# Optimization experiments

Measured on AMD Instinct MI355X. Metric: run time of the kernel, lower is better.

The kernel has to match this reference:

```python
import jax, jax.numpy as jnp
import numpy as np

RATIOS = (0.5, 1.0, 2.0)
SCALES = (8.0, 16.0, 32.0)
FEAT_STRIDE = 16
BASE_SIZE = 16.0
NMS_THRESH = 0.7
N_PRE = 6000   # pre-NMS top-k (eval-mode ProposalCreator default)
N_POST = 300   # post-NMS proposals per image (eval-mode default)
MIN_SIZE = 16.0
SCALE = 1.0


def generate_anchor_base():
    ab = np.zeros((len(RATIOS) * len(SCALES), 4), np.float32)
    for i, r in enumerate(RATIOS):
        for j, s in enumerate(SCALES):
            h = BASE_SIZE * s * np.sqrt(r)
            w = BASE_SIZE * s * np.sqrt(1.0 / r)
            ab[i * len(SCALES) + j] = [-h / 2.0, -w / 2.0, h / 2.0, w / 2.0]
    return jnp.asarray(ab)


def enumerate_shifted_anchor(anchor_base, feat_stride, H, W):
    sy = jnp.arange(H, dtype=jnp.float32) * feat_stride
    sx = jnp.arange(W, dtype=jnp.float32) * feat_stride
    sx, sy = jnp.meshgrid(sx, sy)  # row-major over (y, x), matching torch permute order
    shift = jnp.stack([sy.ravel(), sx.ravel(), sy.ravel(), sx.ravel()], axis=1)  # [K,4]
    anchors = anchor_base[None, :, :] + shift[:, None, :]  # [K, A, 4]
    return anchors.reshape(-1, 4)


def loc2bbox(anchor, loc):
    # boxes in (y1, x1, y2, x2) format
    h = anchor[:, 2] - anchor[:, 0]
    w = anchor[:, 3] - anchor[:, 1]
    cy = anchor[:, 0] + 0.5 * h
    cx = anchor[:, 1] + 0.5 * w
    dy, dx, dh, dw = loc[:, 0], loc[:, 1], loc[:, 2], loc[:, 3]
    cy = cy + dy * h
    cx = cx + dx * w
    h = h * jnp.exp(dh)
    w = w * jnp.exp(dw)
    return jnp.stack([cy - 0.5 * h, cx - 0.5 * w, cy + 0.5 * h, cx + 0.5 * w], axis=1)


def nms_fixed(boxes, scores):
    # boxes [N_PRE,4] sorted desc by scores; greedy NMS emitting N_POST picks (padded)
    area = (boxes[:, 2] - boxes[:, 0]) * (boxes[:, 3] - boxes[:, 1])

    def step(sc, _):
        i = jnp.argmax(sc)
        v = sc[i] > -jnp.inf
        b = boxes[i]
        yy1 = jnp.maximum(boxes[:, 0], b[0])
        xx1 = jnp.maximum(boxes[:, 1], b[1])
        yy2 = jnp.minimum(boxes[:, 2], b[2])
        xx2 = jnp.minimum(boxes[:, 3], b[3])
        inter = jnp.maximum(yy2 - yy1, 0.0) * jnp.maximum(xx2 - xx1, 0.0)
        iou = inter / (area + area[i] - inter + 1e-9)
        sc = jnp.where((iou > NMS_THRESH) & v, -jnp.inf, sc)
        sc = sc.at[i].set(-jnp.inf)
        return sc, (i, v)

    _, (idx, valid) = jax.lax.scan(step, scores, None, length=N_POST)
    return jnp.where(valid[:, None], boxes[idx], 0.0)  # [N_POST, 4]


def proposal_one(loc, score, anchor, img_h, img_w):
    roi = loc2bbox(anchor, loc)
    roi = jnp.stack([
        jnp.clip(roi[:, 0], 0.0, img_h), jnp.clip(roi[:, 1], 0.0, img_w),
        jnp.clip(roi[:, 2], 0.0, img_h), jnp.clip(roi[:, 3], 0.0, img_w)], axis=1)
    hs = roi[:, 2] - roi[:, 0]
    ws = roi[:, 3] - roi[:, 1]
    min_size = MIN_SIZE * SCALE
    valid = (hs >= min_size) & (ws >= min_size)
    s = jnp.where(valid, score, -jnp.inf)
    top_s, top_i = jax.lax.top_k(s, N_PRE)
    return nms_fixed(roi[top_i], top_s)


def setup_inputs() -> dict:
    key = jax.random.key(0)
    ks = jax.random.split(key, 4)
    B, C, H, W = 8, 512, 64, 64
    A = 9
    return {
        "x": jax.random.normal(ks[0], (B, C, H, W), jnp.float32),
        "conv_w": jax.random.normal(ks[1], (C, C, 3, 3), jnp.float32) * 0.01,
        "conv_b": jnp.zeros((C,), jnp.float32),
        "loc_w": jax.random.normal(ks[2], (A * 4, C, 1, 1), jnp.float32) * 0.01,
        "loc_b": jnp.zeros((A * 4,), jnp.float32),
        "cls_w": jax.random.normal(ks[3], (A * 2, C, 1, 1), jnp.float32) * 0.01,
        "cls_b": jnp.zeros((A * 2,), jnp.float32),
        "img_h": 1024,
        "img_w": 1024,
    }


def reference(x, conv_w, conv_b, loc_w, loc_b, cls_w, cls_b, img_h, img_w):
    dn = ("NCHW", "OIHW", "NCHW")
    h = jax.lax.conv_general_dilated(x, conv_w, (1, 1), "SAME", dimension_numbers=dn)
    h = jax.nn.relu(h + conv_b[None, :, None, None])
    cls = jax.nn.sigmoid(
        jax.lax.conv_general_dilated(h, cls_w, (1, 1), "VALID", dimension_numbers=dn)
        + cls_b[None, :, None, None])
    loc = (jax.lax.conv_general_dilated(h, loc_w, (1, 1), "VALID", dimension_numbers=dn)
           + loc_b[None, :, None, None])
    B, _, H, W = h.shape
    anchor = enumerate_shifted_anchor(generate_anchor_base(), FEAT_STRIDE, H, W)
    pred_locations = loc.transpose(0, 2, 3, 1).reshape(B, -1, 4)          # [B, HWA, 4]
    cls_hw = cls.transpose(0, 2, 3, 1)                                     # [B, H, W, 2A]
    objectness = cls_hw.reshape(B, H, W, -1, 2)[..., 1].reshape(B, -1)     # [B, HWA]
    pred_cls_scores = cls_hw.reshape(B, -1, 2)                             # [B, HWA, 2]
    fh = jnp.float32(img_h)
    fw = jnp.float32(img_w)
    rois = jax.vmap(lambda l, s: proposal_one(l, s, anchor, fh, fw))(pred_locations, objectness)
    rois = rois.reshape(B * N_POST, 4)
    roi_indices = jnp.repeat(jnp.arange(B, dtype=jnp.int64 if jax.config.jax_enable_x64 else jnp.int32), N_POST)
    return pred_cls_scores, pred_locations, rois, roi_indices
```

## Files before the change

kernel.cpp:

```cpp
#include <hip/hip_runtime.h>
#include <cstdint>
#include <cmath>


#define AS1U(p) ((const __attribute__((address_space(1))) unsigned int*)(p))
#define AS3U(p) ((__attribute__((address_space(3))) unsigned int*)(p))

typedef float f32x2 __attribute__((ext_vector_type(2)));
typedef float f32x4 __attribute__((ext_vector_type(4)));

__global__ __launch_bounds__(256) void k_wtrans_t(
        const float* __restrict__ w, float* __restrict__ wT) {
    __shared__ float tile[64][65];
    const int cik0 = blockIdx.x * 64;
    const int co0 = blockIdx.y * 64;
    const int t = threadIdx.x;
    const int l = t & 63;
    const int r = t >> 6;
#pragma unroll
    for (int it = 0; it < 16; ++it) {
        const int co_l = r + 4 * it;
        tile[l][co_l] = w[(size_t)(co0 + co_l) * 4608 + cik0 + l];
    }
    __syncthreads();
#pragma unroll
    for (int it = 0; it < 16; ++it) {
        const int cik_l = r + 4 * it;
        wT[(size_t)(cik0 + cik_l) * 512 + co0 + l] = tile[cik_l][l];
    }
}

__global__ __launch_bounds__(256) void k_conv3x3_pk(
        const float* __restrict__ x, const float* __restrict__ wT,
        const float* __restrict__ bias, const float* __restrict__ zeropad,
        float* __restrict__ hout) {
    __shared__ __align__(16) float xs[16][6][68];
    __shared__ __align__(16) float wl[16][9][68];

    const int ytile = blockIdx.x;
    const int co0 = blockIdx.y * 64;
    const int b = blockIdx.z;
    const int t = threadIdx.x;
    const int xq = t & 7;
    const int coq = (t >> 3) & 7;
    const int yy = t >> 6;
    const int lane = t & 63;
    const int y0 = ytile * 4;

    if (t < 96) { int ci = t / 6, ry = t % 6; xs[ci][ry][0] = 0.f; xs[ci][ry][65] = 0.f; }

    f32x2 acc2[4][8];
#pragma unroll
    for (int c = 0; c < 4; ++c)
#pragma unroll
        for (int i = 0; i < 8; ++i) acc2[c][i] = (f32x2){0.f, 0.f};

    const int gy0 = y0 - 1;
    const float* xb = x + ((size_t)b * 512) * 4096;

    for (int ci0 = 0; ci0 < 512; ci0 += 16) {
        __syncthreads();
#pragma unroll
        for (int j = 0; j < 24; ++j) {
            const int ci = 4 * yy + (j / 6);
            const int ry = j % 6;
            const int gy = gy0 + ry;
            const float* src = (gy >= 0 && gy < 64)
                ? xb + ((size_t)(ci0 + ci) * 64 + gy) * 64 + lane
                : zeropad + lane;
            __builtin_amdgcn_global_load_lds(AS1U(src), AS3U(&xs[ci][ry][1]), 4, 0, 0);
        }
#pragma unroll
        for (int c2 = 0; c2 < 4; ++c2) {
            const int cil = 4 * yy + c2;
#pragma unroll
            for (int k = 0; k < 9; ++k) {
                const float* src = wT + ((size_t)(ci0 + cil) * 9 + k) * 512 + co0 + lane;
                __builtin_amdgcn_global_load_lds(AS1U(src), AS3U(&wl[cil][k][0]), 4, 0, 0);
            }
        }
        __syncthreads();
#pragma unroll
        for (int ci = 0; ci < 16; ++ci) {
#pragma unroll
            for (int ky = 0; ky < 3; ++ky) {
                const float* xr = &xs[ci][yy + ky][xq * 8];
                const f32x4 a0 = *(const f32x4*)(xr);
                const f32x4 a1 = *(const f32x4*)(xr + 4);
                const f32x2 a2 = *(const f32x2*)(xr + 8);
                f32x2 xw2[10];
                xw2[0] = (f32x2){a0[0], a0[0]}; xw2[1] = (f32x2){a0[1], a0[1]};
                xw2[2] = (f32x2){a0[2], a0[2]}; xw2[3] = (f32x2){a0[3], a0[3]};
                xw2[4] = (f32x2){a1[0], a1[0]}; xw2[5] = (f32x2){a1[1], a1[1]};
                xw2[6] = (f32x2){a1[2], a1[2]}; xw2[7] = (f32x2){a1[3], a1[3]};
                xw2[8] = (f32x2){a2[0], a2[0]}; xw2[9] = (f32x2){a2[1], a2[1]};
#pragma unroll
                for (int kx = 0; kx < 3; ++kx) {
                    const f32x4 w0 = *(const f32x4*)&wl[ci][ky * 3 + kx][coq * 8];
                    const f32x4 w1 = *(const f32x4*)&wl[ci][ky * 3 + kx][coq * 8 + 4];
                    const f32x2 w00 = (f32x2){w0[0], w0[1]};
                    const f32x2 w01 = (f32x2){w0[2], w0[3]};
                    const f32x2 w10 = (f32x2){w1[0], w1[1]};
                    const f32x2 w11 = (f32x2){w1[2], w1[3]};
#pragma unroll
                    for (int i = 0; i < 8; ++i) {
                        const f32x2 xv2 = xw2[i + kx];
                        acc2[0][i] = __builtin_elementwise_fma(w00, xv2, acc2[0][i]);
                        acc2[1][i] = __builtin_elementwise_fma(w01, xv2, acc2[1][i]);
                        acc2[2][i] = __builtin_elementwise_fma(w10, xv2, acc2[2][i]);
                        acc2[3][i] = __builtin_elementwise_fma(w11, xv2, acc2[3][i]);
                    }
                }
            }
        }
    }
    const int y = y0 + yy;
#pragma unroll
    for (int c = 0; c < 8; ++c) {
        const int co = co0 + coq * 8 + c;
        const float bv = bias[co];
        float* op = hout + (((size_t)b * 512 + co) * 64 + y) * 64 + xq * 8;
        float4 o0, o1;
        o0.x = fmaxf(acc2[c >> 1][0][c & 1] + bv, 0.f);
        o0.y = fmaxf(acc2[c >> 1][1][c & 1] + bv, 0.f);
        o0.z = fmaxf(acc2[c >> 1][2][c & 1] + bv, 0.f);
        o0.w = fmaxf(acc2[c >> 1][3][c & 1] + bv, 0.f);
        o1.x = fmaxf(acc2[c >> 1][4][c & 1] + bv, 0.f);
        o1.y = fmaxf(acc2[c >> 1][5][c & 1] + bv, 0.f);
        o1.z = fmaxf(acc2[c >> 1][6][c & 1] + bv, 0.f);
        o1.w = fmaxf(acc2[c >> 1][7][c & 1] + bv, 0.f);
        *(float4*)(op) = o0;
        *(float4*)(op + 4) = o1;
    }
}

__global__ __launch_bounds__(256) void k_conv3x3(
        const float* __restrict__ x, const float* __restrict__ w,
        const float* __restrict__ bias, const float* __restrict__ zeropad,
        float* __restrict__ hout) {
    __shared__ __align__(16) float xs[8][6][68];
    __shared__ __align__(16) float wl[8][9][68];
    const int ytile = blockIdx.x;
    const int co0 = blockIdx.y * 64;
    const int b = blockIdx.z;
    const int t = threadIdx.x;
    const int xq = t & 7;
    const int coq = (t >> 3) & 7;
    const int yy = t >> 6;
    const int lane = t & 63;
    const int y0 = ytile * 4;
    if (t < 48) { int ci = t / 6, ry = t % 6; xs[ci][ry][0] = 0.f; xs[ci][ry][65] = 0.f; }
    float acc[8][8];
#pragma unroll
    for (int c = 0; c < 8; ++c)
#pragma unroll
        for (int i = 0; i < 8; ++i) acc[c][i] = 0.f;
    const int co_s = t >> 2, qs = t & 3;
    const float* wsrc = w + (size_t)(co0 + co_s) * 4608 + qs * 18;
    float* wrow = &wl[0][0][0] + (size_t)(2 * qs) * 9 * 68 + co_s;
    const int gy0 = y0 - 1;
    const float* xb = x + ((size_t)b * 512) * 4096;
    for (int ci0 = 0; ci0 < 512; ci0 += 8) {
        __syncthreads();
#pragma unroll
        for (int j = 0; j < 12; ++j) {
            const int ci = 2 * yy + (j >= 6 ? 1 : 0);
            const int ry = (j >= 6) ? (j - 6) : j;
            const int gy = gy0 + ry;
            const float* src = (gy >= 0 && gy < 64)
                ? xb + ((size_t)(ci0 + ci) * 64 + gy) * 64 + lane
                : zeropad + lane;
            __builtin_amdgcn_global_load_lds(AS1U(src), AS3U(&xs[ci][ry][1]), 4, 0, 0);
        }
        {
            const float2* wp2 = (const float2*)(wsrc + (size_t)ci0 * 9);
#pragma unroll
            for (int j2 = 0; j2 < 9; ++j2) {
                float2 f = wp2[j2];
                const int i0 = 2 * j2, i1 = 2 * j2 + 1;
                wrow[(i0 < 9 ? 0 : 9 * 68) + (i0 < 9 ? i0 : i0 - 9) * 68] = f.x;
                wrow[(i1 < 9 ? 0 : 9 * 68) + (i1 < 9 ? i1 : i1 - 9) * 68] = f.y;
            }
        }
        __syncthreads();
#pragma unroll
        for (int ci = 0; ci < 8; ++ci) {
#pragma unroll
            for (int ky = 0; ky < 3; ++ky) {
                const float* xr = &xs[ci][yy + ky][xq * 8];
                const float4 a0 = *(const float4*)(xr);
                const float4 a1 = *(const float4*)(xr + 4);
                const float2 a2 = *(const float2*)(xr + 8);
                float xw[10];
                xw[0] = a0.x; xw[1] = a0.y; xw[2] = a0.z; xw[3] = a0.w;
                xw[4] = a1.x; xw[5] = a1.y; xw[6] = a1.z; xw[7] = a1.w;
                xw[8] = a2.x; xw[9] = a2.y;
#pragma unroll
                for (int kx = 0; kx < 3; ++kx) {
                    const float4 w0 = *(const float4*)&wl[ci][ky * 3 + kx][coq * 8];
                    const float4 w1 = *(const float4*)&wl[ci][ky * 3 + kx][coq * 8 + 4];
#pragma unroll
                    for (int i = 0; i < 8; ++i) {
                        const float xv = xw[i + kx];
                        acc[0][i] += w0.x * xv; acc[1][i] += w0.y * xv;
                        acc[2][i] += w0.z * xv; acc[3][i] += w0.w * xv;
                        acc[4][i] += w1.x * xv; acc[5][i] += w1.y * xv;
                        acc[6][i] += w1.z * xv; acc[7][i] += w1.w * xv;
                    }
                }
            }
        }
    }
    const int y = y0 + yy;
#pragma unroll
    for (int c = 0; c < 8; ++c) {
        const int co = co0 + coq * 8 + c;
        const float bv = bias[co];
        float* op = hout + (((size_t)b * 512 + co) * 64 + y) * 64 + xq * 8;
        float4 o0, o1;
        o0.x = fmaxf(acc[c][0] + bv, 0.f); o0.y = fmaxf(acc[c][1] + bv, 0.f);
        o0.z = fmaxf(acc[c][2] + bv, 0.f); o0.w = fmaxf(acc[c][3] + bv, 0.f);
        o1.x = fmaxf(acc[c][4] + bv, 0.f); o1.y = fmaxf(acc[c][5] + bv, 0.f);
        o1.z = fmaxf(acc[c][6] + bv, 0.f); o1.w = fmaxf(acc[c][7] + bv, 0.f);
        *(float4*)(op) = o0;
        *(float4*)(op + 4) = o1;
    }
}

__global__ __launch_bounds__(128) void k_head(
        const float* __restrict__ h,
        const float* __restrict__ cls_w, const float* __restrict__ cls_b,
        const float* __restrict__ loc_w, const float* __restrict__ loc_b,
        const int* __restrict__ img_h_p, const int* __restrict__ img_w_p,
        float* __restrict__ out_cls, float* __restrict__ out_loc,
        float* __restrict__ boxes, float* __restrict__ scores) {
    __shared__ __align__(16) float wAll[128][60];
    const int t = threadIdx.x;
    const int tg = blockIdx.x * 128 + t;
    const int b = tg >> 12;
    const int pos = tg & 4095;
    const int y = pos >> 6, xc = pos & 63;
    f32x2 acc2[27];
#pragma unroll
    for (int p = 0; p < 27; ++p) acc2[p] = (f32x2){0.f, 0.f};
    const float* hp = h + (size_t)b * 2097152 + pos;
    for (int c4 = 0; c4 < 4; ++c4) {
        const int ci0 = c4 * 128;
        __syncthreads();
#pragma unroll
        for (int j = 0; j < 54; ++j) {
            wAll[t][j] = (j < 18) ? cls_w[j * 512 + ci0 + t]
                                  : loc_w[(j - 18) * 512 + ci0 + t];
        }
        __syncthreads();
#pragma unroll 4
        for (int cc = 0; cc < 128; ++cc) {
            const float hv = hp[(size_t)(ci0 + cc) * 4096];
            const f32x2 hv2 = (f32x2){hv, hv};
            const float* wr = &wAll[cc][0];
#pragma unroll
            for (int q = 0; q < 13; ++q) {
                const f32x4 w4 = *(const f32x4*)(wr + 4 * q);
                acc2[2 * q]     = __builtin_elementwise_fma((f32x2){w4[0], w4[1]}, hv2, acc2[2 * q]);
                acc2[2 * q + 1] = __builtin_elementwise_fma((f32x2){w4[2], w4[3]}, hv2, acc2[2 * q + 1]);
            }
            const f32x2 wtl = *(const f32x2*)(wr + 52);
            acc2[26] = __builtin_elementwise_fma(wtl, hv2, acc2[26]);
        }
    }
    float accC[18], accL[36];
#pragma unroll
    for (int o = 0; o < 18; ++o) accC[o] = acc2[o >> 1][o & 1];
#pragma unroll
    for (int l = 0; l < 36; ++l) accL[l] = acc2[9 + (l >> 1)][l & 1];
    const float fh = (float)(*img_h_p);
    const float fw = (float)(*img_w_p);
    {
        const size_t obase = (size_t)b * 73728 + (size_t)pos * 18;
#pragma unroll
        for (int o = 0; o < 18; ++o) {
            accC[o] += cls_b[o];
            out_cls[obase + o] = 1.f / (1.f + expf(-accC[o]));
        }
    }
    {
        const size_t lbase = (size_t)b * 147456 + (size_t)pos * 36;
#pragma unroll
        for (int o = 0; o < 36; ++o) {
            accL[o] += loc_b[o];
            out_loc[lbase + o] = accL[o];
        }
    }
    const float sy = (float)(y * 16), sx = (float)(xc * 16);
    const double RR[3] = {0.5, 1.0, 2.0};
    const double SS[3] = {8.0, 16.0, 32.0};
#pragma unroll
    for (int a = 0; a < 9; ++a) {
        const double r = RR[a / 3], s = SS[a % 3];
        const double hd = 16.0 * s * sqrt(r);
        const double wd = 16.0 * s * sqrt(1.0 / r);
        const float ab0 = (float)(-hd / 2.0), ab1 = (float)(-wd / 2.0);
        const float ab2 = (float)(hd / 2.0), ab3 = (float)(wd / 2.0);
        const float a0 = ab0 + sy, a1 = ab1 + sx, a2 = ab2 + sy, a3 = ab3 + sx;
        float hh = a2 - a0, ww = a3 - a1;
        float cy = a0 + 0.5f * hh, cx = a1 + 0.5f * ww;
        const float dy = accL[a * 4 + 0], dx = accL[a * 4 + 1];
        const float dh = accL[a * 4 + 2], dw = accL[a * 4 + 3];
        cy = cy + dy * hh;
        cx = cx + dx * ww;
        hh = hh * expf(dh);
        ww = ww * expf(dw);
        float y1 = cy - 0.5f * hh, x1 = cx - 0.5f * ww;
        float y2 = cy + 0.5f * hh, x2 = cx + 0.5f * ww;
        y1 = fminf(fmaxf(y1, 0.f), fh); x1 = fminf(fmaxf(x1, 0.f), fw);
        y2 = fminf(fmaxf(y2, 0.f), fh); x2 = fminf(fmaxf(x2, 0.f), fw);
        const bool valid = ((y2 - y1) >= 16.f) && ((x2 - x1) >= 16.f);
        const float sc = 1.f / (1.f + expf(-accC[a * 2 + 1]));
        const int n = pos * 9 + a;
        float* bp = boxes + ((size_t)b * 36864 + n) * 4;
        bp[0] = y1; bp[1] = x1; bp[2] = y2; bp[3] = x2;
        scores[(size_t)b * 36864 + n] = valid ? sc : -INFINITY;
    }
}

__device__ __forceinline__ unsigned fmap(float f) {
    unsigned bits = __float_as_uint(f);
    return ((int)bits < 0) ? ~bits : (bits | 0x80000000u);
}

__global__ __launch_bounds__(1024) void k_select(
        const float* __restrict__ scores, unsigned* __restrict__ sel) {
    __shared__ unsigned h2[16][256];
    __shared__ unsigned hist[256];
    __shared__ unsigned tieL[1024];
    __shared__ unsigned sh_pref, sh_k, sh_cg, sh_ct;
    const int b = blockIdx.x;
    const int t = threadIdx.x;
    const int lane = t & 63;
    const int wid = t >> 6;
    const unsigned long long lmlt = (1ull << lane) - 1ull;
    const float* sp = scores + (size_t)b * 36864;
    unsigned pref = 0;
    unsigned k = 6000;
    for (int p = 3; p >= 0; --p) {
        for (int z = t; z < 4096; z += 1024) ((unsigned*)h2)[z] = 0;
        __syncthreads();
        const int sh = p * 8;
        for (int i4 = t * 4; i4 < 36864; i4 += 4096) {
            const float4 v = *(const float4*)(sp + i4);
            const float vv[4] = {v.x, v.y, v.z, v.w};
#pragma unroll
            for (int e = 0; e < 4; ++e) {
                unsigned u = fmap(vv[e]);
                bool match = (p == 3) || ((u >> (sh + 8)) == (pref >> (sh + 8)));
                if (match) atomicAdd(&h2[wid][(u >> sh) & 255u], 1u);
            }
        }
        __syncthreads();
        if (t < 256) {
            unsigned s = 0;
#pragma unroll
            for (int j = 0; j < 16; ++j) s += h2[j][t];
            hist[t] = s;
        }
        __syncthreads();
        if (t == 0) {
            unsigned c = 0;
            int bsel = 0;
            for (int bin = 255; bin >= 0; --bin) {
                unsigned c2 = c + hist[bin];
                if (c2 >= k) { bsel = bin; k = k - c; break; }
                c = c2;
            }
            pref |= ((unsigned)bsel) << sh;
            sh_pref = pref; sh_k = k;
        }
        __syncthreads();
        pref = sh_pref; k = sh_k;
        __syncthreads();
    }
    if (t == 0) { sh_cg = 0; sh_ct = 0; }
    __syncthreads();
    const unsigned uthr = pref;
    for (int i4 = t * 4; i4 < 36864; i4 += 4096) {
        const float4 v = *(const float4*)(sp + i4);
        const float vv[4] = {v.x, v.y, v.z, v.w};
#pragma unroll
        for (int e = 0; e < 4; ++e) {
            const int i = i4 + e;
            unsigned u = fmap(vv[e]);
            const bool g = (u > uthr);
            const bool eq = (u == uthr);
            unsigned long long bg = __ballot(g);
            if (bg) {
                int lead = __ffsll((unsigned long long)bg) - 1;
                unsigned basev = 0;
                if (lane == lead) basev = atomicAdd(&sh_cg, (unsigned)__popcll(bg));
                basev = __shfl(basev, lead, 64);
                if (g) sel[(size_t)b * 6000 + basev + (unsigned)__popcll(bg & lmlt)] = (unsigned)i;
            }
            unsigned long long be = __ballot(eq);
            if (be) {
                int lead = __ffsll((unsigned long long)be) - 1;
                unsigned baset = 0;
                if (lane == lead) baset = atomicAdd(&sh_ct, (unsigned)__popcll(be));
                baset = __shfl(baset, lead, 64);
                if (eq) {
                    unsigned tp = baset + (unsigned)__popcll(be & lmlt);
                    if (tp < 1024) tieL[tp] = (unsigned)i;
                }
            }
        }
    }
    __syncthreads();
    const unsigned G = sh_cg;
    const unsigned T = sh_ct;
    const unsigned need = k;
    const unsigned Tc = T < 1024u ? T : 1024u;
    if ((unsigned)t >= Tc) tieL[t] = 0xFFFFFFFFu;
    __syncthreads();
    if (need > 0) {
        if (T > 1) {
            for (int kk = 2; kk <= 1024; kk <<= 1) {
                for (int j = kk >> 1; j > 0; j >>= 1) {
                    int ixj = t ^ j;
                    if (ixj > t) {
                        unsigned va = tieL[t], vb = tieL[ixj];
                        bool up = ((t & kk) == 0);
                        if (up ? (va > vb) : (va < vb)) { tieL[t] = vb; tieL[ixj] = va; }
                    }
                    __syncthreads();
                }
            }
        }
        if ((unsigned)t < need) sel[(size_t)b * 6000 + G + t] = tieL[t];
    }
}

__global__ __launch_bounds__(1024) void k_nms(
        const float* __restrict__ boxes, const float* __restrict__ scores,
        const unsigned* __restrict__ sel,
        float* __restrict__ rois, float* __restrict__ roi_idx) {
    __shared__ unsigned long long warr[2][16];
    __shared__ float wbox[2][16][4];
    const int b = blockIdx.x;
    const int t = threadIdx.x;
    const unsigned UNEG = 0x007FFFFFu;
    float bx[6][4];
    unsigned long long key[6];
#pragma unroll
    for (int j = 0; j < 6; ++j) {
        int s = t + j * 1024;
        if (s < 6000) {
            unsigned idx = sel[(size_t)b * 6000 + s];
            const float* bp = boxes + ((size_t)b * 36864 + idx) * 4;
            bx[j][0] = bp[0]; bx[j][1] = bp[1]; bx[j][2] = bp[2]; bx[j][3] = bp[3];
            unsigned u = fmap(scores[(size_t)b * 36864 + idx]);
            key[j] = ((unsigned long long)u << 32) | (unsigned)(~idx);
        } else {
            key[j] = 0ull;
            bx[j][0] = bx[j][1] = bx[j][2] = bx[j][3] = 0.f;
        }
    }
    const int lane = t & 63;
    const int wid = t >> 6;
    float* orow = rois + (size_t)b * 300 * 4;
    for (int k = 0; k < 300; ++k) {
        const int pb = k & 1;
        unsigned long long m = key[0];
        float b0 = bx[0][0], b1 = bx[0][1], b2 = bx[0][2], b3 = bx[0][3];
#pragma unroll
        for (int j = 1; j < 6; ++j) {
            if (key[j] > m) { m = key[j]; b0 = bx[j][0]; b1 = bx[j][1]; b2 = bx[j][2]; b3 = bx[j][3]; }
        }
        const unsigned long long lm = m;
#pragma unroll
        for (int d = 32; d > 0; d >>= 1) {
            unsigned long long o = __shfl_xor(m, d, 64);
            if (o > m) m = o;
        }
        unsigned long long own = __ballot(lm == m);
        if (lane == __ffsll(own) - 1) {
            warr[pb][wid] = m;
            wbox[pb][wid][0] = b0; wbox[pb][wid][1] = b1;
            wbox[pb][wid][2] = b2; wbox[pb][wid][3] = b3;
        }
        __syncthreads();
        unsigned long long wk = warr[pb][0];
        int wm = 0;
#pragma unroll
        for (int i = 1; i < 16; ++i) {
            unsigned long long v = warr[pb][i];
            if (v > wk) { wk = v; wm = i; }
        }
        const unsigned uhi = (unsigned)(wk >> 32);
        if (uhi > UNEG) {
            const float py1 = wbox[pb][wm][0], px1 = wbox[pb][wm][1];
            const float py2 = wbox[pb][wm][2], px2 = wbox[pb][wm][3];
            const float parea = (py2 - py1) * (px2 - px1);
            if (t == 0) {
                orow[k * 4 + 0] = py1; orow[k * 4 + 1] = px1;
                orow[k * 4 + 2] = py2; orow[k * 4 + 3] = px2;
                roi_idx[b * 300 + k] = (float)b;
            }
#pragma unroll
            for (int j = 0; j < 6; ++j) {
                if ((unsigned)(key[j] >> 32) > UNEG) {
                    float yy1 = fmaxf(bx[j][0], py1);
                    float xx1 = fmaxf(bx[j][1], px1);
                    float yy2 = fminf(bx[j][2], py2);
                    float xx2 = fminf(bx[j][3], px2);
                    float inter = fmaxf(yy2 - yy1, 0.f) * fmaxf(xx2 - xx1, 0.f);
                    float area = (bx[j][2] - bx[j][0]) * (bx[j][3] - bx[j][1]);
                    float iou = inter / (area + parea - inter + 1e-9f);
                    if (iou > 0.7f)
                        key[j] = ((unsigned long long)UNEG << 32) | (key[j] & 0xFFFFFFFFull);
                }
            }
        } else {
            if (t == 0) {
                orow[k * 4 + 0] = 0.f; orow[k * 4 + 1] = 0.f;
                orow[k * 4 + 2] = 0.f; orow[k * 4 + 3] = 0.f;
                roi_idx[b * 300 + k] = (float)b;
            }
        }
    }
}

extern "C" void kernel_launch(void* const* d_in, const int* in_sizes, int n_in,
                              void* d_out, int out_size, void* d_ws, size_t ws_size,
                              hipStream_t stream) {
    (void)in_sizes; (void)n_in; (void)out_size;
    const float* x      = (const float*)d_in[0];
    const float* conv_w = (const float*)d_in[1];
    const float* conv_b = (const float*)d_in[2];
    const float* loc_w  = (const float*)d_in[3];
    const float* loc_b  = (const float*)d_in[4];
    const float* cls_w  = (const float*)d_in[5];
    const float* cls_b  = (const float*)d_in[6];
    const int* img_h    = (const int*)d_in[7];
    const int* img_w    = (const int*)d_in[8];

    char* ws = (char*)d_ws;
    float*    h      = (float*)(ws + 0);
    float*    boxes  = (float*)(ws + 67108864);
    float*    scores = (float*)(ws + 71827456);
    unsigned* sel    = (unsigned*)(ws + 73007104);
    float*    zp     = (float*)(ws + 73199104);
    float*    wT     = (float*)(ws + 73199360);

    float* out      = (float*)d_out;
    float* out_cls  = out;
    float* out_loc  = out + 589824;
    float* rois     = out + 1769472;
    float* ridx     = out + 1779072;

    const bool big_ws = (ws_size >= 82636544ull);

    hipMemsetAsync(zp, 0, 256, stream);
    if (big_ws) {
        k_wtrans_t<<<dim3(72, 8), 256, 0, stream>>>(conv_w, wT);
        k_conv3x3_pk<<<dim3(16, 8, 8), 256, 0, stream>>>(x, wT, conv_b, zp, h);
    } else {
        k_conv3x3<<<dim3(16, 8, 8), 256, 0, stream>>>(x, conv_w, conv_b, zp, h);
    }
    k_head<<<dim3(256), 128, 0, stream>>>(h, cls_w, cls_b, loc_w, loc_b,
                                          img_h, img_w, out_cls, out_loc, boxes, scores);
    k_select<<<dim3(8), 1024, 0, stream>>>(scores, sel);
    k_nms<<<dim3(8), 1024, 0, stream>>>(boxes, scores, sel, rois, ridx);
}
```

Measured before the change: 2.906 ms.

## Halve conv input-channel tile and fuse top-k selection with NMS kernel

The 3x3 conv kernel now stages 8 input channels per iteration instead of 16, which halves shared memory per block and may allow more resident blocks, at the cost of twice as many barriers and load rounds. Separately, the top-k select and NMS kernels are merged into one, keeping the selected index list in shared memory. This removes a kernel launch and a global round-trip for the selection buffer.

New measurement: 2.888 ms. Within noise of the previous version (-0.6%).

```diff
diff --git a/kernel.cpp b/kernel.cpp
--- a/kernel.cpp
+++ b/kernel.cpp
@@ -34,8 +34,8 @@
         const float* __restrict__ x, const float* __restrict__ wT,
         const float* __restrict__ bias, const float* __restrict__ zeropad,
         float* __restrict__ hout) {
-    __shared__ __align__(16) float xs[16][6][68];
-    __shared__ __align__(16) float wl[16][9][68];
+    __shared__ __align__(16) float xs[8][6][68];
+    __shared__ __align__(16) float wl[8][9][68];
 
     const int ytile = blockIdx.x;
     const int co0 = blockIdx.y * 64;
@@ -47,7 +47,7 @@
     const int lane = t & 63;
     const int y0 = ytile * 4;
 
-    if (t < 96) { int ci = t / 6, ry = t % 6; xs[ci][ry][0] = 0.f; xs[ci][ry][65] = 0.f; }
+    if (t < 48) { int ci = t / 6, ry = t % 6; xs[ci][ry][0] = 0.f; xs[ci][ry][65] = 0.f; }
 
     f32x2 acc2[4][8];
 #pragma unroll
@@ -58,12 +58,12 @@
     const int gy0 = y0 - 1;
     const float* xb = x + ((size_t)b * 512) * 4096;
 
-    for (int ci0 = 0; ci0 < 512; ci0 += 16) {
-        __syncthreads();
-#pragma unroll
-        for (int j = 0; j < 24; ++j) {
-            const int ci = 4 * yy + (j / 6);
-            const int ry = j % 6;
+    for (int ci0 = 0; ci0 < 512; ci0 += 8) {
+        __syncthreads();
+#pragma unroll
+        for (int j = 0; j < 12; ++j) {
+            const int ci = 2 * yy + (j >= 6 ? 1 : 0);
+            const int ry = (j >= 6) ? (j - 6) : j;
             const int gy = gy0 + ry;
             const float* src = (gy >= 0 && gy < 64)
                 ? xb + ((size_t)(ci0 + ci) * 64 + gy) * 64 + lane
@@ -71,8 +71,8 @@
             __builtin_amdgcn_global_load_lds(AS1U(src), AS3U(&xs[ci][ry][1]), 4, 0, 0);
         }
 #pragma unroll
-        for (int c2 = 0; c2 < 4; ++c2) {
-            const int cil = 4 * yy + c2;
+        for (int c2 = 0; c2 < 2; ++c2) {
+            const int cil = 2 * yy + c2;
 #pragma unroll
             for (int k = 0; k < 9; ++k) {
                 const float* src = wT + ((size_t)(ci0 + cil) * 9 + k) * 512 + co0 + lane;
@@ -81,7 +81,7 @@
         }
         __syncthreads();
 #pragma unroll
-        for (int ci = 0; ci < 16; ++ci) {
+        for (int ci = 0; ci < 8; ++ci) {
 #pragma unroll
             for (int ky = 0; ky < 3; ++ky) {
                 const float* xr = &xs[ci][yy + ky][xq * 8];
@@ -328,11 +328,15 @@
     return ((int)bits < 0) ? ~bits : (bits | 0x80000000u);
 }
 
-__global__ __launch_bounds__(1024) void k_select(
-        const float* __restrict__ scores, unsigned* __restrict__ sel) {
+__global__ __launch_bounds__(1024) void k_selnms(
+        const float* __restrict__ scores, const float* __restrict__ boxes,
+        float* __restrict__ rois, float* __restrict__ roi_idx) {
     __shared__ unsigned h2[16][256];
     __shared__ unsigned hist[256];
     __shared__ unsigned tieL[1024];
+    __shared__ unsigned selL[6000];
+    __shared__ unsigned long long warr[2][16];
+    __shared__ float wbox[2][16][4];
     __shared__ unsigned sh_pref, sh_k, sh_cg, sh_ct;
     const int b = blockIdx.x;
     const int t = threadIdx.x;
@@ -340,6 +344,7 @@
     const int wid = t >> 6;
     const unsigned long long lmlt = (1ull << lane) - 1ull;
     const float* sp = scores + (size_t)b * 36864;
+
     unsigned pref = 0;
     unsigned k = 6000;
     for (int p = 3; p >= 0; --p) {
@@ -397,7 +402,7 @@
                 unsigned basev = 0;
                 if (lane == lead) basev = atomicAdd(&sh_cg, (unsigned)__popcll(bg));
                 basev = __shfl(basev, lead, 64);
-                if (g) sel[(size_t)b * 6000 + basev + (unsigned)__popcll(bg & lmlt)] = (unsigned)i;
+                if (g) selL[basev + (unsigned)__popcll(bg & lmlt)] = (unsigned)i;
             }
             unsigned long long be = __ballot(eq);
             if (be) {
@@ -433,18 +438,10 @@
                 }
             }
         }
-        if ((unsigned)t < need) sel[(size_t)b * 6000 + G + t] = tieL[t];
-    }
-}
-
-__global__ __launch_bounds__(1024) void k_nms(
-        const float* __restrict__ boxes, const float* __restrict__ scores,
-        const unsigned* __restrict__ sel,
-        float* __restrict__ rois, float* __restrict__ roi_idx) {
-    __shared__ unsigned long long warr[2][16];
-    __shared__ float wbox[2][16][4];
-    const int b = blockIdx.x;
-    const int t = threadIdx.x;
+        if ((unsigned)t < need) selL[G + t] = tieL[t];
+    }
+    __syncthreads();
+
     const unsigned UNEG = 0x007FFFFFu;
     float bx[6][4];
     unsigned long long key[6];
@@ -452,21 +449,19 @@
     for (int j = 0; j < 6; ++j) {
         int s = t + j * 1024;
         if (s < 6000) {
-            unsigned idx = sel[(size_t)b * 6000 + s];
+            unsigned idx = selL[s];
             const float* bp = boxes + ((size_t)b * 36864 + idx) * 4;
             bx[j][0] = bp[0]; bx[j][1] = bp[1]; bx[j][2] = bp[2]; bx[j][3] = bp[3];
-            unsigned u = fmap(scores[(size_t)b * 36864 + idx]);
+            unsigned u = fmap(sp[idx]);
             key[j] = ((unsigned long long)u << 32) | (unsigned)(~idx);
         } else {
             key[j] = 0ull;
             bx[j][0] = bx[j][1] = bx[j][2] = bx[j][3] = 0.f;
         }
     }
-    const int lane = t & 63;
-    const int wid = t >> 6;
     float* orow = rois + (size_t)b * 300 * 4;
-    for (int k = 0; k < 300; ++k) {
-        const int pb = k & 1;
+    for (int k2 = 0; k2 < 300; ++k2) {
+        const int pb = k2 & 1;
         unsigned long long m = key[0];
         float b0 = bx[0][0], b1 = bx[0][1], b2 = bx[0][2], b3 = bx[0][3];
 #pragma unroll
@@ -499,9 +494,9 @@
             const float py2 = wbox[pb][wm][2], px2 = wbox[pb][wm][3];
             const float parea = (py2 - py1) * (px2 - px1);
             if (t == 0) {
-                orow[k * 4 + 0] = py1; orow[k * 4 + 1] = px1;
-                orow[k * 4 + 2] = py2; orow[k * 4 + 3] = px2;
-                roi_idx[b * 300 + k] = (float)b;
+                orow[k2 * 4 + 0] = py1; orow[k2 * 4 + 1] = px1;
+                orow[k2 * 4 + 2] = py2; orow[k2 * 4 + 3] = px2;
+                roi_idx[b * 300 + k2] = (float)b;
             }
 #pragma unroll
             for (int j = 0; j < 6; ++j) {
@@ -519,9 +514,9 @@
             }
         } else {
             if (t == 0) {
-                orow[k * 4 + 0] = 0.f; orow[k * 4 + 1] = 0.f;
-                orow[k * 4 + 2] = 0.f; orow[k * 4 + 3] = 0.f;
-                roi_idx[b * 300 + k] = (float)b;
+                orow[k2 * 4 + 0] = 0.f; orow[k2 * 4 + 1] = 0.f;
+                orow[k2 * 4 + 2] = 0.f; orow[k2 * 4 + 3] = 0.f;
+                roi_idx[b * 300 + k2] = (float)b;
             }
         }
     }
@@ -545,7 +540,6 @@
     float*    h      = (float*)(ws + 0);
     float*    boxes  = (float*)(ws + 67108864);
     float*    scores = (float*)(ws + 71827456);
-    unsigned* sel    = (unsigned*)(ws + 73007104);
     float*    zp     = (float*)(ws + 73199104);
     float*    wT     = (float*)(ws + 73199360);
 
@@ -566,6 +560,5 @@
     }
     k_head<<<dim3(256), 128, 0, stream>>>(h, cls_w, cls_b, loc_w, loc_b,
                                           img_h, img_w, out_cls, out_loc, boxes, scores);
-    k_select<<<dim3(8), 1024, 0, stream>>>(scores, sel);
-    k_nms<<<dim3(8), 1024, 0, stream>>>(boxes, scores, sel, rois, ridx);
-}
+    k_selnms<<<dim3(8), 1024, 0, stream>>>(scores, boxes, rois, ridx);
+}
```
